# Kernel optimization log

Hardware: AMD Instinct MI355X
Metric: run time of the kernel (lower is better)

## Reference

```python
import jax, jax.numpy as jnp
import numpy as np

L, B, S, H, HD, NL = 13, 16, 512, 768, 32, 3


def _gru_final(x, Wi, Uh, b, reverse):
    """Keras GRU (reset_after=True) final state. x: [N, T, H] -> [N, HD]."""
    n = x.shape[0]
    hd = Uh.shape[0]
    # precompute input projections for all timesteps: [T, N, 3*HD]
    xp = jnp.einsum('nth,hk->tnk', x, Wi) + b[0]

    def step(h, xt):
        rec = h @ Uh + b[1]
        xz, xr, xh = jnp.split(xt, 3, axis=-1)
        rz, rr, rh = jnp.split(rec, 3, axis=-1)
        z = jax.nn.sigmoid(xz + rz)
        r = jax.nn.sigmoid(xr + rr)
        hh = jnp.tanh(xh + r * rh)
        return z * h + (1.0 - z) * hh, None

    h0 = jnp.zeros((n, hd), x.dtype)
    h, _ = jax.lax.scan(step, h0, xp, reverse=reverse)
    return h


def setup_inputs() -> dict:
    key = jax.random.key(0)
    ks = jax.random.split(key, 9)
    s_in = 1.0 / np.sqrt(H)
    s_rec = 1.0 / np.sqrt(HD)
    return {
        'hidden_states': jax.random.normal(ks[0], (L, B, S, H), jnp.float32),
        'Wi_f': jax.random.normal(ks[1], (H, 3 * HD), jnp.float32) * s_in,
        'Uh_f': jax.random.normal(ks[2], (HD, 3 * HD), jnp.float32) * s_rec,
        'b_f': jnp.zeros((2, 3 * HD), jnp.float32),
        'Wi_b': jax.random.normal(ks[3], (H, 3 * HD), jnp.float32) * s_in,
        'Uh_b': jax.random.normal(ks[4], (HD, 3 * HD), jnp.float32) * s_rec,
        'b_b': jnp.zeros((2, 3 * HD), jnp.float32),
        'W_lin': jax.random.normal(ks[5], (HD, H), jnp.float32) * s_rec,
        'b_lin': jnp.zeros((H,), jnp.float32),
        'W_cls': jax.random.normal(ks[6], (H, NL), jnp.float32) * s_in,
        'b_cls': jnp.zeros((NL,), jnp.float32),
    }


def reference(hidden_states, Wi_f, Uh_f, b_f, Wi_b, Uh_b, b_b, W_lin, b_lin, W_cls, b_cls):
    nl, nb, ns, nh = hidden_states.shape
    # [L,B,S,H] -> [B*S, L, H]: GRU runs over the layer axis, batched over all tokens
    x = jnp.transpose(hidden_states, (1, 2, 0, 3)).reshape(nb * ns, nl, nh)
    h_fw = _gru_final(x, Wi_f, Uh_f, b_f, reverse=False)
    h_bw = _gru_final(x, Wi_b, Uh_b, b_b, reverse=True)
    last_correction = (h_fw + h_bw).reshape(nb, ns, -1)  # Add()(states)
    corrected = hidden_states[-1] + jnp.tanh(last_correction @ W_lin + b_lin)
    pooled = corrected.mean(axis=1)  # GlobalAveragePooling1D
    return jax.nn.softmax(pooled @ W_cls + b_cls, axis=-1)
```

## Files before the change

kernel.cpp:

```cpp
#include <hip/hip_runtime.h>
#include <hip/hip_bf16.h>
#include <math.h>

#define LL 13
#define BB 16
#define SS 512
#define HH 768
#define HDD 32
#define NN (BB*SS)
#define NT (LL*NN)

typedef __bf16 bf16x4 __attribute__((ext_vector_type(4)));
typedef __bf16 bf16x8 __attribute__((ext_vector_type(8)));
typedef float  f32x4  __attribute__((ext_vector_type(4)));

__device__ __forceinline__ float sigmoid_f(float x) {
    return 1.f / (1.f + __expf(-x));
}
__device__ __forceinline__ float tanh_fast(float x) {
    float ax = fabsf(x);
    float e  = __expf(-2.f * ax);
    float t  = (1.f - e) / (1.f + e);
    return copysignf(t, x);
}

__global__ __launch_bounds__(256) void k_prep(
    const float* __restrict__ Wf, const float* __restrict__ Wb,
    __bf16* __restrict__ Bt)
{
    int idx = blockIdx.x * 256 + threadIdx.x;
    if (idx >= 192 * 768) return;
    int col = idx / 768, k = idx - col * 768;
    float v = (col < 96) ? Wf[(size_t)k * 96 + col]
                         : Wb[(size_t)k * 96 + col - 96];
    Bt[idx] = (__bf16)v;
}

#define BMp 128
#define BKp 32
__global__ __launch_bounds__(256) void k_projm(
    const float* __restrict__ A, const __bf16* __restrict__ Bt,
    const float* __restrict__ bfv, const float* __restrict__ bbv,
    float* __restrict__ xpf, float* __restrict__ xpb)
{
    __shared__ __bf16 Al[BMp * 40];
    __shared__ __bf16 Bl[192 * 40];

    const int t    = threadIdx.x;
    const int r0   = blockIdx.x * BMp;
    const int wave = t >> 6, lane = t & 63;
    const int wm   = wave >> 1;
    const int wn   = wave & 1;
    const int lr   = lane & 15;
    const int lg   = lane >> 4;

    f32x4 acc[4][6];
    #pragma unroll
    for (int m = 0; m < 4; ++m)
        #pragma unroll
        for (int n = 0; n < 6; ++n)
            acc[m][n] = (f32x4){0.f, 0.f, 0.f, 0.f};

    for (int k0 = 0; k0 < HH; k0 += BKp) {
        #pragma unroll
        for (int i = 0; i < 4; ++i) {
            int f = i * 256 + t;
            int row = f >> 3, c4 = f & 7;
            float4 av = *(const float4*)(A + (size_t)(r0 + row) * HH + k0 + c4 * 4);
            bf16x4 bv;
            bv[0] = (__bf16)av.x; bv[1] = (__bf16)av.y;
            bv[2] = (__bf16)av.z; bv[3] = (__bf16)av.w;
            *(bf16x4*)(&Al[row * 40 + c4 * 4]) = bv;
        }
        #pragma unroll
        for (int i = 0; i < 3; ++i) {
            int f = i * 256 + t;
            int col = f >> 2, c8 = f & 3;
            bf16x8 bv = *(const bf16x8*)(Bt + (size_t)col * HH + k0 + c8 * 8);
            *(bf16x8*)(&Bl[col * 40 + c8 * 8]) = bv;
        }
        __syncthreads();

        bf16x8 af[4], bfr[6];
        #pragma unroll
        for (int m = 0; m < 4; ++m)
            af[m] = *(const bf16x8*)(&Al[(wm * 64 + m * 16 + lr) * 40 + lg * 8]);
        #pragma unroll
        for (int n = 0; n < 6; ++n)
            bfr[n] = *(const bf16x8*)(&Bl[(wn * 96 + n * 16 + lr) * 40 + lg * 8]);
        #pragma unroll
        for (int m = 0; m < 4; ++m)
            #pragma unroll
            for (int n = 0; n < 6; ++n)
                acc[m][n] = __builtin_amdgcn_mfma_f32_16x16x32_bf16(
                    af[m], bfr[n], acc[m][n], 0, 0, 0);
        __syncthreads();
    }

    const float* bsrc = wn ? bbv : bfv;
    float*       dst  = wn ? xpb : xpf;
    float bias[6];
    #pragma unroll
    for (int n = 0; n < 6; ++n) bias[n] = bsrc[n * 16 + lr];
    #pragma unroll
    for (int m = 0; m < 4; ++m) {
        #pragma unroll
        for (int j = 0; j < 4; ++j) {
            size_t row = (size_t)(r0 + wm * 64 + m * 16 + lg * 4 + j);
            #pragma unroll
            for (int n = 0; n < 6; ++n)
                dst[row * 96 + n * 16 + lr] = acc[m][n][j] + bias[n];
        }
    }
}

__global__ __launch_bounds__(256) void k_gru32(
    const float* __restrict__ xpf, const float* __restrict__ xpb,
    const float* __restrict__ Uf, const float* __restrict__ Ub,
    const float* __restrict__ bf_, const float* __restrict__ bb_,
    float* __restrict__ lcf, float* __restrict__ lcb)
{
    const int rev = blockIdx.y;
    const float* xp = rev ? xpb : xpf;
    const float* U  = rev ? Ub  : Uf;
    const float* bi = rev ? bb_ : bf_;
    float*      lco = rev ? lcb : lcf;

    const int t   = threadIdx.x;
    const int j   = t & 31;
    const int seq = blockIdx.x * 8 + (t >> 5);

    float Uz[32], Ur[32], Uh_[32];
    #pragma unroll
    for (int m = 0; m < 32; ++m) {
        Uz[m]  = U[m * 96 + j];
        Ur[m]  = U[m * 96 + 32 + j];
        Uh_[m] = U[m * 96 + 64 + j];
    }
    const float bz = bi[96 + j], br = bi[128 + j], bh = bi[160 + j];

    float h = 0.f;
    #pragma unroll 1
    for (int s = 0; s < LL; ++s) {
        const int tt = rev ? (LL - 1 - s) : s;
        const float* xr_ = xp + ((size_t)tt * NN + seq) * 96;
        float xz = xr_[j], xr = xr_[32 + j], xh = xr_[64 + j];
        float rz = bz, rr = br, rh = bh;
        #pragma unroll
        for (int m = 0; m < 32; ++m) {
            float hm = __shfl(h, m, 32);
            rz = fmaf(hm, Uz[m], rz);
            rr = fmaf(hm, Ur[m], rr);
            rh = fmaf(hm, Uh_[m], rh);
        }
        float z  = sigmoid_f(xz + rz);
        float r  = sigmoid_f(xr + rr);
        float hh = tanh_fast(xh + r * rh);
        h = z * h + (1.f - z) * hh;
    }
    lco[(size_t)seq * 32 + j] = h;
}

__global__ __launch_bounds__(256) void k_corr(
    const float* __restrict__ hs_last, const float* __restrict__ lcf,
    const float* __restrict__ lcb, const float* __restrict__ Wlin,
    const float* __restrict__ blin, float* __restrict__ partial)
{
    __shared__ float lcl[32 * 32];
    const int t  = threadIdx.x;
    const int b  = blockIdx.x;
    const int sc = blockIdx.y;
    const int s0 = sc * 32;

    for (int i = t; i < 32 * 32; i += 256) {
        size_t idx = ((size_t)b * SS + s0) * 32 + i;
        lcl[i] = lcf[idx] + lcb[idx];
    }
    __syncthreads();

    float Wc[32][3];
    #pragma unroll
    for (int jj = 0; jj < 32; ++jj) {
        Wc[jj][0] = Wlin[(size_t)jj * HH + t];
        Wc[jj][1] = Wlin[(size_t)jj * HH + t + 256];
        Wc[jj][2] = Wlin[(size_t)jj * HH + t + 512];
    }
    const float bl0 = blin[t], bl1 = blin[t + 256], bl2 = blin[t + 512];

    float acc0 = 0.f, acc1 = 0.f, acc2 = 0.f;
    #pragma unroll 1
    for (int s = 0; s < 32; ++s) {
        float v0 = bl0, v1 = bl1, v2 = bl2;
        #pragma unroll
        for (int jj = 0; jj < 32; ++jj) {
            const float l = lcl[s * 32 + jj];
            v0 = fmaf(l, Wc[jj][0], v0);
            v1 = fmaf(l, Wc[jj][1], v1);
            v2 = fmaf(l, Wc[jj][2], v2);
        }
        const float* hp = hs_last + ((size_t)b * SS + s0 + s) * HH;
        acc0 += hp[t]       + tanh_fast(v0);
        acc1 += hp[t + 256] + tanh_fast(v1);
        acc2 += hp[t + 512] + tanh_fast(v2);
    }
    float* pp = partial + ((size_t)b * 16 + sc) * HH;
    pp[t] = acc0; pp[t + 256] = acc1; pp[t + 512] = acc2;
}

__global__ __launch_bounds__(256) void k_final(
    const float* __restrict__ partial, const float* __restrict__ Wcls,
    const float* __restrict__ bcls, float* __restrict__ out)
{
    __shared__ float pooled[16 * HH];
    __shared__ float logits[48];
    const int t = threadIdx.x;
    for (int i = t; i < 16 * HH; i += 256) {
        int b = i / HH, h = i - b * HH;
        float s = 0.f;
        #pragma unroll
        for (int c = 0; c < 16; ++c) s += partial[((size_t)b * 16 + c) * HH + h];
        pooled[i] = s * (1.f / (float)SS);
    }
    __syncthreads();
    if (t < 48) {
        int b = t / 3, c = t - (t / 3) * 3;
        float s = bcls[c];
        for (int h = 0; h < HH; ++h)
            s = fmaf(pooled[b * HH + h], Wcls[h * 3 + c], s);
        logits[t] = s;
    }
    __syncthreads();
    if (t < 16) {
        float l0 = logits[t * 3], l1 = logits[t * 3 + 1], l2 = logits[t * 3 + 2];
        float m = fmaxf(l0, fmaxf(l1, l2));
        float e0 = __expf(l0 - m), e1 = __expf(l1 - m), e2 = __expf(l2 - m);
        float inv = 1.f / (e0 + e1 + e2);
        out[t * 3 + 0] = e0 * inv;
        out[t * 3 + 1] = e1 * inv;
        out[t * 3 + 2] = e2 * inv;
    }
}

extern "C" void kernel_launch(void* const* d_in, const int* in_sizes, int n_in,
                              void* d_out, int out_size, void* d_ws, size_t ws_size,
                              hipStream_t stream)
{
    const float* hs    = (const float*)d_in[0];
    const float* Wi_f  = (const float*)d_in[1];
    const float* Uh_f  = (const float*)d_in[2];
    const float* b_f   = (const float*)d_in[3];
    const float* Wi_b  = (const float*)d_in[4];
    const float* Uh_b  = (const float*)d_in[5];
    const float* b_b   = (const float*)d_in[6];
    const float* W_lin = (const float*)d_in[7];
    const float* b_lin = (const float*)d_in[8];
    const float* W_cls = (const float*)d_in[9];
    const float* b_cls = (const float*)d_in[10];

    float* ws      = (float*)d_ws;
    float* xpf     = ws;
    float* xpb     = xpf + (size_t)NT * 96;
    float* lcf     = xpb + (size_t)NT * 96;
    float* lcb     = lcf + (size_t)NN * 32;
    float* partial = lcb + (size_t)NN * 32;
    __bf16* Bt     = (__bf16*)partial;
    float* out     = (float*)d_out;

    k_prep<<<(192 * 768 + 255) / 256, 256, 0, stream>>>(Wi_f, Wi_b, Bt);
    k_projm<<<NT / BMp, 256, 0, stream>>>(hs, Bt, b_f, b_b, xpf, xpb);
    k_gru32<<<dim3(NN * 32 / 256, 2), 256, 0, stream>>>(xpf, xpb, Uh_f, Uh_b,
                                                        b_f, b_b, lcf, lcb);
    k_corr<<<dim3(16, 16), 256, 0, stream>>>(hs + (size_t)12 * NN * HH, lcf, lcb,
                                             W_lin, b_lin, partial);
    k_final<<<1, 256, 0, stream>>>(partial, W_cls, b_cls, out);
}
```

Baseline: 590.8 us.

## Prefetch next K-tile into registers in projection GEMM and next step in GRU

The projection GEMM now loads the next K-slice of A and B into registers right after the barrier, so global loads overlap with the MFMA work on the current tile. Before, it loaded synchronously before each LDS store. The GRU recurrence kernel likewise loads the next timestep's input projections before computing the current step, hiding global latency behind the shuffle/FMA chain. This costs extra registers, which may reduce occupancy.

```diff
diff --git a/kernel.cpp b/kernel.cpp
--- a/kernel.cpp
+++ b/kernel.cpp
@@ -54,6 +54,11 @@
     const int lr   = lane & 15;
     const int lg   = lane >> 4;
 
+    const int arow = t >> 3, ac4 = t & 7;
+    const int bcol = t >> 2, bc8 = t & 3;
+    const float*  Aip = A  + (size_t)(r0 + arow) * HH + ac4 * 4;
+    const __bf16* Bip = Bt + (size_t)bcol * HH + bc8 * 8;
+
     f32x4 acc[4][6];
     #pragma unroll
     for (int m = 0; m < 4; ++m)
@@ -61,25 +66,36 @@
         for (int n = 0; n < 6; ++n)
             acc[m][n] = (f32x4){0.f, 0.f, 0.f, 0.f};
 
+    float4 avr[4];
+    bf16x8 bvr[3];
+    #pragma unroll
+    for (int i = 0; i < 4; ++i)
+        avr[i] = *(const float4*)(Aip + (size_t)i * 32 * HH);
+    #pragma unroll
+    for (int i = 0; i < 3; ++i)
+        bvr[i] = *(const bf16x8*)(Bip + (size_t)i * 64 * HH);
+
     for (int k0 = 0; k0 < HH; k0 += BKp) {
         #pragma unroll
         for (int i = 0; i < 4; ++i) {
-            int f = i * 256 + t;
-            int row = f >> 3, c4 = f & 7;
-            float4 av = *(const float4*)(A + (size_t)(r0 + row) * HH + k0 + c4 * 4);
             bf16x4 bv;
-            bv[0] = (__bf16)av.x; bv[1] = (__bf16)av.y;
-            bv[2] = (__bf16)av.z; bv[3] = (__bf16)av.w;
-            *(bf16x4*)(&Al[row * 40 + c4 * 4]) = bv;
-        }
-        #pragma unroll
-        for (int i = 0; i < 3; ++i) {
-            int f = i * 256 + t;
-            int col = f >> 2, c8 = f & 3;
-            bf16x8 bv = *(const bf16x8*)(Bt + (size_t)col * HH + k0 + c8 * 8);
-            *(bf16x8*)(&Bl[col * 40 + c8 * 8]) = bv;
-        }
+            bv[0] = (__bf16)avr[i].x; bv[1] = (__bf16)avr[i].y;
+            bv[2] = (__bf16)avr[i].z; bv[3] = (__bf16)avr[i].w;
+            *(bf16x4*)(&Al[(i * 32 + arow) * 40 + ac4 * 4]) = bv;
+        }
+        #pragma unroll
+        for (int i = 0; i < 3; ++i)
+            *(bf16x8*)(&Bl[(i * 64 + bcol) * 40 + bc8 * 8]) = bvr[i];
         __syncthreads();
+
+        if (k0 + BKp < HH) {
+            #pragma unroll
+            for (int i = 0; i < 4; ++i)
+                avr[i] = *(const float4*)(Aip + (k0 + BKp) + (size_t)i * 32 * HH);
+            #pragma unroll
+            for (int i = 0; i < 3; ++i)
+                bvr[i] = *(const bf16x8*)(Bip + (k0 + BKp) + (size_t)i * 64 * HH);
+        }
 
         bf16x8 af[4], bfr[6];
         #pragma unroll
@@ -140,11 +156,18 @@
     const float bz = bi[96 + j], br = bi[128 + j], bh = bi[160 + j];
 
     float h = 0.f;
+    const int tt0 = rev ? (LL - 1) : 0;
+    const float* xq = xp + ((size_t)tt0 * NN + seq) * 96;
+    float xz = xq[j], xr = xq[32 + j], xh = xq[64 + j];
+
     #pragma unroll 1
     for (int s = 0; s < LL; ++s) {
-        const int tt = rev ? (LL - 1 - s) : s;
-        const float* xr_ = xp + ((size_t)tt * NN + seq) * 96;
-        float xz = xr_[j], xr = xr_[32 + j], xh = xr_[64 + j];
+        float nz = 0.f, nr = 0.f, nh = 0.f;
+        if (s + 1 < LL) {
+            const int tn = rev ? (LL - 2 - s) : (s + 1);
+            const float* xn = xp + ((size_t)tn * NN + seq) * 96;
+            nz = xn[j]; nr = xn[32 + j]; nh = xn[64 + j];
+        }
         float rz = bz, rr = br, rh = bh;
         #pragma unroll
         for (int m = 0; m < 32; ++m) {
@@ -153,10 +176,11 @@
             rr = fmaf(hm, Ur[m], rr);
             rh = fmaf(hm, Uh_[m], rh);
         }
-        float z  = sigmoid_f(xz + rz);
-        float r  = sigmoid_f(xr + rr);
-        float hh = tanh_fast(xh + r * rh);
-        h = z * h + (1.f - z) * hh;
+        float z   = sigmoid_f(xz + rz);
+        float r   = sigmoid_f(xr + rr);
+        float hhv = tanh_fast(xh + r * rh);
+        h = z * h + (1.f - z) * hhv;
+        xz = nz; xr = nr; xh = nh;
     }
     lco[(size_t)seq * 32 + j] = h;
 }
```

New measurement: 589.7 us. About the same (-0.2%).
